# Kernel optimization log

Measured on AMD Instinct MI355X. Metric: run time of the kernel, lower is better.

The kernel has to match this reference:

```python
import jax, jax.numpy as jnp
import numpy as np

B, S, D_MODEL, H = 2, 2048, 768, 12
HD = D_MODEL // H  # head_dim = 64
EPS = 1e-5


def setup_inputs() -> dict:
    key = jax.random.key(0)
    ks = jax.random.split(key, 5)
    sc = 0.02
    return {
        "x": jax.random.normal(ks[0], (B, S, D_MODEL), dtype=jnp.float32),
        "Wproj_w": jax.random.normal(ks[1], (7 * D_MODEL, D_MODEL), dtype=jnp.float32) * sc,
        "Wproj_b": jax.random.normal(ks[2], (7 * D_MODEL,), dtype=jnp.float32) * sc,
        "gn_w": jnp.ones((D_MODEL,), dtype=jnp.float32),
        "gn_b": jnp.zeros((D_MODEL,), dtype=jnp.float32),
        "out_w": jax.random.normal(ks[3], (D_MODEL, D_MODEL), dtype=jnp.float32) * sc,
        "out_b": jax.random.normal(ks[4], (D_MODEL,), dtype=jnp.float32) * sc,
    }


def _time_swiglu(qkv):
    # qkv: [B, S, 7, H, D]
    q1, k1, q2, k2, q3, k3, v = [qkv[:, :, i] for i in range(7)]
    a1 = jnp.einsum('bthd,bshd->bhts', q1, k1)  # [B,H,S,S], raw scores, no softmax
    a2 = jnp.einsum('bthd,bshd->bhts', q2, k2)
    a3 = jnp.einsum('bthd,bshd->bhts', q3, k3)
    t1 = jax.nn.silu(jnp.einsum('bhts,bshd->bthd', a1, v))
    t2 = jnp.einsum('bhts,bshd->bthd', a2, v)
    return jnp.einsum('bhts,bshd->bthd', a3, t1 * t2)  # [B,S,H,D]


def _group_norm(ctx, gn_w, gn_b):
    # ctx: [B, S, D_MODEL]; torch applies GroupNorm(H, D_MODEL) over (B, C=D_MODEL, L=S)
    g = ctx.reshape(B, S, H, HD)
    mean = jnp.mean(g, axis=(1, 3), keepdims=True)          # per (batch, group) over (S, HD)
    var = jnp.var(g, axis=(1, 3), keepdims=True)
    g = (g - mean) * jax.lax.rsqrt(var + EPS)
    g = g.reshape(B, S, D_MODEL)
    return g * gn_w + gn_b


def reference(x, Wproj_w, Wproj_b, gn_w, gn_b, out_w, out_b):
    qkv = x @ Wproj_w.T + Wproj_b                  # [B,S,7*D_MODEL]
    qkv = qkv.reshape(B, S, 7, H, HD)
    ctx = _time_swiglu(qkv).reshape(B, S, D_MODEL)  # [B,S,D_MODEL]
    ctx = _group_norm(ctx, gn_w, gn_b)
    return ctx @ out_w.T + out_b
```

## Files before the change

kernel.cpp:

```cpp
#include <hip/hip_runtime.h>
#include <hip/hip_bf16.h>
#include <stdint.h>

typedef short short8 __attribute__((ext_vector_type(8)));
typedef float f32x4 __attribute__((ext_vector_type(4)));
typedef float f32x16 __attribute__((ext_vector_type(16)));
typedef unsigned short u16x4 __attribute__((ext_vector_type(4)));
typedef unsigned uint4v __attribute__((ext_vector_type(4)));

#define MFMA16 __builtin_amdgcn_mfma_f32_16x16x32_bf16
#define MFMA32 __builtin_amdgcn_mfma_f32_32x32x16_bf16

typedef unsigned int __attribute__((address_space(1))) as1_u32;
typedef unsigned int __attribute__((address_space(3))) as3_u32;
#define GLOAD16(gsrc, ldst) \
  __builtin_amdgcn_global_load_lds((const as1_u32*)(gsrc), (as3_u32*)(ldst), 16, 0, 0)

__device__ __forceinline__ unsigned short f2bf(float f) {
  __hip_bfloat16 h = __float2bfloat16(f);
  return *(unsigned short*)&h;
}
__device__ __forceinline__ unsigned pk2(float lo, float hi) {
  return ((unsigned)f2bf(hi) << 16) | (unsigned)f2bf(lo);
}
__device__ __forceinline__ void plswap(unsigned &a, unsigned &b) {
  asm volatile("v_permlane32_swap_b32 %0, %1" : "+v"(a), "+v"(b));
}

__device__ __forceinline__ short8 pv_frag(const f32x16* acc, int kc2) {
  int n = kc2 >> 1, c = kc2 & 1;
  int o0 = 2 * c, o1 = 2 * c + 1;
  unsigned x0 = pk2(acc[n][o0 * 4 + 0], acc[n][o0 * 4 + 1]);
  unsigned x1 = pk2(acc[n][o0 * 4 + 2], acc[n][o0 * 4 + 3]);
  unsigned y0 = pk2(acc[n][o1 * 4 + 0], acc[n][o1 * 4 + 1]);
  unsigned y1 = pk2(acc[n][o1 * 4 + 2], acc[n][o1 * 4 + 3]);
  plswap(x0, y0);
  plswap(x1, y1);
  uint4v fu; fu.x = x0; fu.y = x1; fu.z = y0; fu.w = y1;
  return __builtin_bit_cast(short8, fu);
}

__global__ __launch_bounds__(256) void cvt_bf16_4(const float* __restrict__ in,
                                                  unsigned short* __restrict__ out,
                                                  int n) {
  int i = (blockIdx.x * 256 + threadIdx.x) * 4;
  if (i >= n) return;
  f32x4 v = *(const f32x4*)(in + i);
  u16x4 o;
  o.x = f2bf(v.x); o.y = f2bf(v.y); o.z = f2bf(v.z); o.w = f2bf(v.w);
  *(u16x4*)(out + i) = o;
}

__global__ __launch_bounds__(256) void transp64(const unsigned short* __restrict__ src,
                                                int stride, int off,
                                                unsigned short* __restrict__ dst) {
  __shared__ __align__(16) unsigned short t[64 * 64];
  const int tid = threadIdx.x;
  const int tt = blockIdx.x, bh = blockIdx.y;
  const int b = bh / 12, h = bh % 12;
  const unsigned short* sbase = src + (size_t)(b * 2048 + tt * 64) * stride + h * 64 + off;
  for (int it = 0; it < 2; ++it) {
    int slot = it * 256 + tid, s = slot >> 3, j = slot & 7;
    short8 v = *(const short8*)(sbase + (size_t)s * stride + j * 8);
    int phys = (s + 8 * j) & 63;
    for (int e = 0; e < 8; ++e)
      t[(j * 8 + e) * 64 + phys] = ((unsigned short*)&v)[e];
  }
  __syncthreads();
  unsigned short* dbase = dst + (size_t)bh * 64 * 2048 + tt * 64;
  for (int it = 0; it < 2; ++it) {
    int slot = it * 256 + tid, d = slot >> 3, c = slot & 7;
    int pc = (c + (d >> 3)) & 7;
    short8 v = *(const short8*)(t + d * 64 + pc * 8);
    *(short8*)(dbase + (size_t)d * 2048 + c * 8) = v;
  }
}

template <bool OUT_BF16>
__global__ __launch_bounds__(256) void gemm_nt(const unsigned short* __restrict__ A,
                                               const unsigned short* __restrict__ Bm,
                                               const float* __restrict__ bias,
                                               void* __restrict__ Cout,
                                               int M, int N, int K) {
  __shared__ __align__(16) char smem[32768];
  char* As = smem;
  char* Bs = smem + 16384;
  const int tid = threadIdx.x;
  const int w = tid >> 6, l = tid & 63;
  const int wm = w >> 1, wn = w & 1;
  const int Row0 = blockIdx.y * 128, Col0 = blockIdx.x * 128;

  f32x4 z; z.x = 0.f; z.y = 0.f; z.z = 0.f; z.w = 0.f;
  f32x4 acc[4][4];
  for (int m = 0; m < 4; ++m)
    for (int n = 0; n < 4; ++n) acc[m][n] = z;

  for (int k0 = 0; k0 < K; k0 += 64) {
    for (int it = 0; it < 4; ++it) {
      int slot = it * 256 + tid;
      int row = slot >> 3, j = slot & 7;
      int gc = j ^ (row & 7);
      GLOAD16(A + (size_t)(Row0 + row) * K + k0 + gc * 8, As + slot * 16);
      GLOAD16(Bm + (size_t)(Col0 + row) * K + k0 + gc * 8, Bs + slot * 16);
    }
    __syncthreads();
    for (int kc = 0; kc < 2; ++kc) {
      int c = (l >> 4) + 4 * kc;
      short8 af[4], bf[4];
      for (int m = 0; m < 4; ++m) {
        int t = wm * 64 + m * 16 + (l & 15);
        af[m] = *(const short8*)(As + t * 128 + ((c ^ (t & 7)) * 16));
      }
      for (int n = 0; n < 4; ++n) {
        int t = wn * 64 + n * 16 + (l & 15);
        bf[n] = *(const short8*)(Bs + t * 128 + ((c ^ (t & 7)) * 16));
      }
      for (int m = 0; m < 4; ++m)
        for (int n = 0; n < 4; ++n)
          acc[m][n] = MFMA16(af[m], bf[n], acc[m][n], 0, 0, 0);
    }
    __syncthreads();
  }
  for (int n = 0; n < 4; ++n) {
    int col = Col0 + wn * 64 + n * 16 + (l & 15);
    float bv = bias[col];
    for (int m = 0; m < 4; ++m) {
      int rbase = Row0 + wm * 64 + m * 16 + (l >> 4) * 4;
      for (int r = 0; r < 4; ++r) {
        float v = acc[m][n][r] + bv;
        size_t idx = (size_t)(rbase + r) * N + col;
        if (OUT_BF16) ((unsigned short*)Cout)[idx] = f2bf(v);
        else          ((float*)Cout)[idx] = v;
      }
    }
  }
}

__global__ __launch_bounds__(256) void pass1(const unsigned short* __restrict__ qkv,
                                             const unsigned short* __restrict__ vt,
                                             unsigned short* __restrict__ u) {
  __shared__ __align__(16) char smem[24576];
  char* K1s = smem;
  char* K2s = smem + 8192;
  char* Vts = smem + 16384;
  const int tid = threadIdx.x, w = tid >> 6, l = tid & 63;
  const int g5 = l >> 5, l31 = l & 31;
  const int tt = blockIdx.x, bh = blockIdx.y;
  const int b = bh / 12, h = bh % 12;

  const int tg = tt * 128 + w * 32 + l31;
  const unsigned short* qrow = qkv + (size_t)(b * 2048 + tg) * 5376 + h * 64;
  short8 q1f[4], q2f[4];
#pragma unroll
  for (int kc = 0; kc < 4; ++kc) {
    int d = kc * 16 + g5 * 8;
    q1f[kc] = *(const short8*)(qrow + 0 * 768 + d);
    q2f[kc] = *(const short8*)(qrow + 2 * 768 + d);
  }

  f32x16 z16;
#pragma unroll
  for (int i = 0; i < 16; ++i) z16[i] = 0.f;
  f32x16 t1a[2], t2a[2];
  t1a[0] = z16; t1a[1] = z16; t2a[0] = z16; t2a[1] = z16;

  for (int s0 = 0; s0 < 2048; s0 += 64) {
#pragma unroll
    for (int it = 0; it < 2; ++it) {
      int slot = it * 256 + tid;
      int row = slot >> 3, j = slot & 7;
      int gc = j ^ (row & 7);
      const unsigned short* ksrc =
          qkv + (size_t)(b * 2048 + s0 + row) * 5376 + h * 64 + 768 + gc * 8;
      GLOAD16(ksrc, K1s + slot * 16);
      GLOAD16(ksrc + 2 * 768, K2s + slot * 16);
      GLOAD16(vt + (size_t)(bh * 64 + row) * 2048 + s0 + gc * 8, Vts + slot * 16);
    }
    __syncthreads();

    f32x16 a1t[2], a2t[2];
    a1t[0] = z16; a1t[1] = z16; a2t[0] = z16; a2t[1] = z16;
#pragma unroll
    for (int kc = 0; kc < 4; ++kc) {
#pragma unroll
      for (int n = 0; n < 2; ++n) {
        int srow = n * 32 + l31;
        int off = srow * 128 + (((kc * 2 + g5) ^ (l31 & 7)) * 16);
        a1t[n] = MFMA32(*(const short8*)(K1s + off), q1f[kc], a1t[n], 0, 0, 0);
        a2t[n] = MFMA32(*(const short8*)(K2s + off), q2f[kc], a2t[n], 0, 0, 0);
      }
    }

#pragma unroll
    for (int kc2 = 0; kc2 < 4; ++kc2) {
      short8 pa1 = pv_frag(a1t, kc2);
      short8 pa2 = pv_frag(a2t, kc2);
#pragma unroll
      for (int dn = 0; dn < 2; ++dn) {
        int drow = dn * 32 + l31;
        short8 vf = *(const short8*)(Vts + drow * 128 + (((kc2 * 2 + g5) ^ (l31 & 7)) * 16));
        t1a[dn] = MFMA32(pa1, vf, t1a[dn], 0, 0, 0);
        t2a[dn] = MFMA32(pa2, vf, t2a[dn], 0, 0, 0);
      }
    }
    __syncthreads();
  }

#pragma unroll
  for (int dn = 0; dn < 2; ++dn)
#pragma unroll
    for (int r = 0; r < 16; ++r) {
      int t = tt * 128 + w * 32 + (r & 3) + 8 * (r >> 2) + 4 * g5;
      int d = dn * 32 + l31;
      float x1 = t1a[dn][r], x2 = t2a[dn][r];
      float uu = (x1 / (1.f + expf(-x1))) * x2;
      u[(size_t)(b * 2048 + t) * 768 + h * 64 + d] = f2bf(uu);
    }
}

__global__ __launch_bounds__(256) void pass2(const unsigned short* __restrict__ qkv,
                                             const unsigned short* __restrict__ ut,
                                             float* __restrict__ ctx,
                                             float* __restrict__ partials) {
  __shared__ __align__(16) char smem[16384];
  char* K3s = smem;
  char* Uts = smem + 8192;
  const int tid = threadIdx.x, w = tid >> 6, l = tid & 63;
  const int g5 = l >> 5, l31 = l & 31;
  const int tt = blockIdx.x, bh = blockIdx.y;
  const int b = bh / 12, h = bh % 12;

  const int tg = tt * 128 + w * 32 + l31;
  const unsigned short* qrow = qkv + (size_t)(b * 2048 + tg) * 5376 + h * 64;
  short8 q3f[4];
#pragma unroll
  for (int kc = 0; kc < 4; ++kc)
    q3f[kc] = *(const short8*)(qrow + 4 * 768 + kc * 16 + g5 * 8);

  f32x16 z16;
#pragma unroll
  for (int i = 0; i < 16; ++i) z16[i] = 0.f;
  f32x16 ca[2];
  ca[0] = z16; ca[1] = z16;

  for (int s0 = 0; s0 < 2048; s0 += 64) {
#pragma unroll
    for (int it = 0; it < 2; ++it) {
      int slot = it * 256 + tid;
      int row = slot >> 3, j = slot & 7;
      int gc = j ^ (row & 7);
      GLOAD16(qkv + (size_t)(b * 2048 + s0 + row) * 5376 + h * 64 + 5 * 768 + gc * 8,
              K3s + slot * 16);
      GLOAD16(ut + (size_t)(bh * 64 + row) * 2048 + s0 + gc * 8, Uts + slot * 16);
    }
    __syncthreads();

    f32x16 a3t[2];
    a3t[0] = z16; a3t[1] = z16;
#pragma unroll
    for (int kc = 0; kc < 4; ++kc) {
#pragma unroll
      for (int n = 0; n < 2; ++n) {
        int srow = n * 32 + l31;
        int off = srow * 128 + (((kc * 2 + g5) ^ (l31 & 7)) * 16);
        a3t[n] = MFMA32(*(const short8*)(K3s + off), q3f[kc], a3t[n], 0, 0, 0);
      }
    }
#pragma unroll
    for (int kc2 = 0; kc2 < 4; ++kc2) {
      short8 pa = pv_frag(a3t, kc2);
#pragma unroll
      for (int dn = 0; dn < 2; ++dn) {
        int drow = dn * 32 + l31;
        short8 uf = *(const short8*)(Uts + drow * 128 + (((kc2 * 2 + g5) ^ (l31 & 7)) * 16));
        ca[dn] = MFMA32(pa, uf, ca[dn], 0, 0, 0);
      }
    }
    __syncthreads();
  }

  float psum = 0.f, psum2 = 0.f;
#pragma unroll
  for (int dn = 0; dn < 2; ++dn)
#pragma unroll
    for (int r = 0; r < 16; ++r) {
      int t = tt * 128 + w * 32 + (r & 3) + 8 * (r >> 2) + 4 * g5;
      int d = dn * 32 + l31;
      float v = ca[dn][r];
      ctx[(size_t)(b * 2048 + t) * 768 + h * 64 + d] = v;
      psum += v; psum2 += v * v;
    }

  float* red = (float*)smem;
  red[tid] = psum; red[256 + tid] = psum2;
  __syncthreads();
  for (int st = 128; st > 0; st >>= 1) {
    if (tid < st) {
      red[tid] += red[tid + st];
      red[256 + tid] += red[256 + tid + st];
    }
    __syncthreads();
  }
  if (tid == 0) {
    partials[(bh * 16 + tt) * 2] = red[0];
    partials[(bh * 16 + tt) * 2 + 1] = red[256];
  }
}

__global__ __launch_bounds__(64) void gn_finalize(const float* __restrict__ partials,
                                                  float* __restrict__ stats) {
  const int g = blockIdx.x;
  const int l = threadIdx.x;
  double s = 0.0, s2 = 0.0;
  if (l < 16) {
    s = (double)partials[(g * 16 + l) * 2];
    s2 = (double)partials[(g * 16 + l) * 2 + 1];
  }
  for (int off = 32; off > 0; off >>= 1) {
    s += __shfl_down(s, off, 64);
    s2 += __shfl_down(s2, off, 64);
  }
  if (l == 0) {
    const double N = 2048.0 * 64.0;
    double mean = s / N;
    double var = s2 / N - mean * mean;
    stats[g * 2] = (float)mean;
    stats[g * 2 + 1] = (float)(1.0 / sqrt(var + 1e-5));
  }
}

__global__ __launch_bounds__(256) void gn_apply(const float* __restrict__ ctx,
                                                const float* __restrict__ stats,
                                                const float* __restrict__ gw,
                                                const float* __restrict__ gb,
                                                unsigned short* __restrict__ outc) {
  int i = blockIdx.x * 256 + threadIdx.x;
  if (i >= 4096 * 768) return;
  int c = i % 768;
  int b = i / (2048 * 768);
  int g = b * 12 + (c >> 6);
  float v = (ctx[i] - stats[2 * g]) * stats[2 * g + 1];
  outc[i] = f2bf(v * gw[c] + gb[c]);
}

extern "C" void kernel_launch(void* const* d_in, const int* in_sizes, int n_in,
                              void* d_out, int out_size, void* d_ws, size_t ws_size,
                              hipStream_t stream) {
  const float* x   = (const float*)d_in[0];
  const float* Wpw = (const float*)d_in[1];
  const float* Wpb = (const float*)d_in[2];
  const float* gnw = (const float*)d_in[3];
  const float* gnb = (const float*)d_in[4];
  const float* ow  = (const float*)d_in[5];
  const float* ob  = (const float*)d_in[6];
  float* out = (float*)d_out;

  char* ws = (char*)d_ws;
  size_t off = 0;
  auto carve = [&](size_t bytes) {
    char* p = ws + off;
    off = (off + bytes + 255) & ~(size_t)255;
    return p;
  };
  unsigned short* xb   = (unsigned short*)carve((size_t)4096 * 768 * 2);
  unsigned short* wb   = (unsigned short*)carve((size_t)5376 * 768 * 2);
  unsigned short* owb  = (unsigned short*)carve((size_t)768 * 768 * 2);
  unsigned short* qkvb = (unsigned short*)carve((size_t)4096 * 5376 * 2);
  unsigned short* ub   = (unsigned short*)carve((size_t)4096 * 768 * 2);
  unsigned short* vtb  = (unsigned short*)carve((size_t)24 * 64 * 2048 * 2);
  unsigned short* utb  = (unsigned short*)carve((size_t)24 * 64 * 2048 * 2);
  float* ctx           = (float*)carve((size_t)4096 * 768 * 4);
  float* partials      = (float*)carve(24 * 16 * 2 * 4);
  float* stats         = (float*)carve(48 * 4);

  cvt_bf16_4<<<3072, 256, 0, stream>>>(x, xb, 4096 * 768);
  cvt_bf16_4<<<4032, 256, 0, stream>>>(Wpw, wb, 5376 * 768);
  cvt_bf16_4<<<576, 256, 0, stream>>>(ow, owb, 768 * 768);

  gemm_nt<true><<<dim3(42, 32), 256, 0, stream>>>(xb, wb, Wpb, qkvb, 4096, 5376, 768);
  transp64<<<dim3(32, 24), 256, 0, stream>>>(qkvb, 5376, 6 * 768, vtb);
  pass1<<<dim3(16, 24), 256, 0, stream>>>(qkvb, vtb, ub);
  transp64<<<dim3(32, 24), 256, 0, stream>>>(ub, 768, 0, utb);
  pass2<<<dim3(16, 24), 256, 0, stream>>>(qkvb, utb, ctx, partials);
  gn_finalize<<<24, 64, 0, stream>>>(partials, stats);
  gn_apply<<<12288, 256, 0, stream>>>(ctx, stats, gnw, gnb, xb);
  gemm_nt<false><<<dim3(6, 32), 256, 0, stream>>>(xb, owb, ob, out, 4096, 768, 768);
}
```

Before: 233.3 us.

## Split sequence reduction across two wave groups in pass1 and pass2

Doubles the block size of the two attention passes to 512 threads. Each half of the block processes one half of the key/sequence range with its own LDS staging buffers, and the partial accumulators are then combined through shared memory before the epilogue. The grid has only 384 blocks, so this is meant to put more waves per CU and hide latency on the long serial s-loop. The cost is extra LDS use, more barriers, an accumulator merge step, and half the waves sitting idle during the epilogue.

```diff
diff --git a/kernel.cpp b/kernel.cpp
--- a/kernel.cpp
+++ b/kernel.cpp
@@ -136,19 +136,21 @@
   }
 }
 
-__global__ __launch_bounds__(256) void pass1(const unsigned short* __restrict__ qkv,
-                                             const unsigned short* __restrict__ vt,
-                                             unsigned short* __restrict__ u) {
-  __shared__ __align__(16) char smem[24576];
-  char* K1s = smem;
-  char* K2s = smem + 8192;
-  char* Vts = smem + 16384;
+__global__ __launch_bounds__(512, 4) void pass1(const unsigned short* __restrict__ qkv,
+                                                const unsigned short* __restrict__ vt,
+                                                unsigned short* __restrict__ u) {
+  __shared__ __align__(16) char smem[49152];
   const int tid = threadIdx.x, w = tid >> 6, l = tid & 63;
+  const int sh = w >> 2, wi = w & 3;
+  const int tidh = tid & 255;
   const int g5 = l >> 5, l31 = l & 31;
   const int tt = blockIdx.x, bh = blockIdx.y;
   const int b = bh / 12, h = bh % 12;
-
-  const int tg = tt * 128 + w * 32 + l31;
+  char* K1s = smem + sh * 24576;
+  char* K2s = K1s + 8192;
+  char* Vts = K1s + 16384;
+
+  const int tg = tt * 128 + wi * 32 + l31;
   const unsigned short* qrow = qkv + (size_t)(b * 2048 + tg) * 5376 + h * 64;
   short8 q1f[4], q2f[4];
 #pragma unroll
@@ -164,10 +166,11 @@
   f32x16 t1a[2], t2a[2];
   t1a[0] = z16; t1a[1] = z16; t2a[0] = z16; t2a[1] = z16;
 
-  for (int s0 = 0; s0 < 2048; s0 += 64) {
+  for (int si = 0; si < 16; ++si) {
+    const int s0 = sh * 1024 + si * 64;
 #pragma unroll
     for (int it = 0; it < 2; ++it) {
-      int slot = it * 256 + tid;
+      int slot = it * 256 + tidh;
       int row = slot >> 3, j = slot & 7;
       int gc = j ^ (row & 7);
       const unsigned short* ksrc =
@@ -206,31 +209,79 @@
     __syncthreads();
   }
 
-#pragma unroll
-  for (int dn = 0; dn < 2; ++dn)
-#pragma unroll
-    for (int r = 0; r < 16; ++r) {
-      int t = tt * 128 + w * 32 + (r & 3) + 8 * (r >> 2) + 4 * g5;
-      int d = dn * 32 + l31;
-      float x1 = t1a[dn][r], x2 = t2a[dn][r];
-      float uu = (x1 / (1.f + expf(-x1))) * x2;
-      u[(size_t)(b * 2048 + t) * 768 + h * 64 + d] = f2bf(uu);
-    }
-}
-
-__global__ __launch_bounds__(256) void pass2(const unsigned short* __restrict__ qkv,
-                                             const unsigned short* __restrict__ ut,
-                                             float* __restrict__ ctx,
-                                             float* __restrict__ partials) {
-  __shared__ __align__(16) char smem[16384];
-  char* K3s = smem;
-  char* Uts = smem + 8192;
+  char* comb = smem + wi * 8192;
+  if (sh == 1) {
+#pragma unroll
+    for (int c = 0; c < 8; ++c) {
+      f32x4 q;
+      q.x = t1a[c >> 2][(c & 3) * 4 + 0];
+      q.y = t1a[c >> 2][(c & 3) * 4 + 1];
+      q.z = t1a[c >> 2][(c & 3) * 4 + 2];
+      q.w = t1a[c >> 2][(c & 3) * 4 + 3];
+      *(f32x4*)(comb + c * 1024 + l * 16) = q;
+    }
+  }
+  __syncthreads();
+  if (sh == 0) {
+#pragma unroll
+    for (int c = 0; c < 8; ++c) {
+      f32x4 q = *(const f32x4*)(comb + c * 1024 + l * 16);
+      t1a[c >> 2][(c & 3) * 4 + 0] += q.x;
+      t1a[c >> 2][(c & 3) * 4 + 1] += q.y;
+      t1a[c >> 2][(c & 3) * 4 + 2] += q.z;
+      t1a[c >> 2][(c & 3) * 4 + 3] += q.w;
+    }
+  }
+  __syncthreads();
+  if (sh == 1) {
+#pragma unroll
+    for (int c = 0; c < 8; ++c) {
+      f32x4 q;
+      q.x = t2a[c >> 2][(c & 3) * 4 + 0];
+      q.y = t2a[c >> 2][(c & 3) * 4 + 1];
+      q.z = t2a[c >> 2][(c & 3) * 4 + 2];
+      q.w = t2a[c >> 2][(c & 3) * 4 + 3];
+      *(f32x4*)(comb + c * 1024 + l * 16) = q;
+    }
+  }
+  __syncthreads();
+  if (sh == 0) {
+#pragma unroll
+    for (int c = 0; c < 8; ++c) {
+      f32x4 q = *(const f32x4*)(comb + c * 1024 + l * 16);
+      t2a[c >> 2][(c & 3) * 4 + 0] += q.x;
+      t2a[c >> 2][(c & 3) * 4 + 1] += q.y;
+      t2a[c >> 2][(c & 3) * 4 + 2] += q.z;
+      t2a[c >> 2][(c & 3) * 4 + 3] += q.w;
+    }
+#pragma unroll
+    for (int dn = 0; dn < 2; ++dn)
+#pragma unroll
+      for (int r = 0; r < 16; ++r) {
+        int t = tt * 128 + wi * 32 + (r & 3) + 8 * (r >> 2) + 4 * g5;
+        int d = dn * 32 + l31;
+        float x1 = t1a[dn][r], x2 = t2a[dn][r];
+        float uu = (x1 / (1.f + expf(-x1))) * x2;
+        u[(size_t)(b * 2048 + t) * 768 + h * 64 + d] = f2bf(uu);
+      }
+  }
+}
+
+__global__ __launch_bounds__(512, 4) void pass2(const unsigned short* __restrict__ qkv,
+                                                const unsigned short* __restrict__ ut,
+                                                float* __restrict__ ctx,
+                                                float* __restrict__ partials) {
+  __shared__ __align__(16) char smem[32768];
   const int tid = threadIdx.x, w = tid >> 6, l = tid & 63;
+  const int sh = w >> 2, wi = w & 3;
+  const int tidh = tid & 255;
   const int g5 = l >> 5, l31 = l & 31;
   const int tt = blockIdx.x, bh = blockIdx.y;
   const int b = bh / 12, h = bh % 12;
-
-  const int tg = tt * 128 + w * 32 + l31;
+  char* K3s = smem + sh * 16384;
+  char* Uts = K3s + 8192;
+
+  const int tg = tt * 128 + wi * 32 + l31;
   const unsigned short* qrow = qkv + (size_t)(b * 2048 + tg) * 5376 + h * 64;
   short8 q3f[4];
 #pragma unroll
@@ -243,10 +294,11 @@
   f32x16 ca[2];
   ca[0] = z16; ca[1] = z16;
 
-  for (int s0 = 0; s0 < 2048; s0 += 64) {
+  for (int si = 0; si < 16; ++si) {
+    const int s0 = sh * 1024 + si * 64;
 #pragma unroll
     for (int it = 0; it < 2; ++it) {
-      int slot = it * 256 + tid;
+      int slot = it * 256 + tidh;
       int row = slot >> 3, j = slot & 7;
       int gc = j ^ (row & 7);
       GLOAD16(qkv + (size_t)(b * 2048 + s0 + row) * 5376 + h * 64 + 5 * 768 + gc * 8,
@@ -279,31 +331,55 @@
     __syncthreads();
   }
 
+  char* comb = smem + wi * 8192;
+  if (sh == 1) {
+#pragma unroll
+    for (int c = 0; c < 8; ++c) {
+      f32x4 q;
+      q.x = ca[c >> 2][(c & 3) * 4 + 0];
+      q.y = ca[c >> 2][(c & 3) * 4 + 1];
+      q.z = ca[c >> 2][(c & 3) * 4 + 2];
+      q.w = ca[c >> 2][(c & 3) * 4 + 3];
+      *(f32x4*)(comb + c * 1024 + l * 16) = q;
+    }
+  }
+  __syncthreads();
   float psum = 0.f, psum2 = 0.f;
-#pragma unroll
-  for (int dn = 0; dn < 2; ++dn)
-#pragma unroll
-    for (int r = 0; r < 16; ++r) {
-      int t = tt * 128 + w * 32 + (r & 3) + 8 * (r >> 2) + 4 * g5;
-      int d = dn * 32 + l31;
-      float v = ca[dn][r];
-      ctx[(size_t)(b * 2048 + t) * 768 + h * 64 + d] = v;
-      psum += v; psum2 += v * v;
-    }
+  if (sh == 0) {
+#pragma unroll
+    for (int c = 0; c < 8; ++c) {
+      f32x4 q = *(const f32x4*)(comb + c * 1024 + l * 16);
+      ca[c >> 2][(c & 3) * 4 + 0] += q.x;
+      ca[c >> 2][(c & 3) * 4 + 1] += q.y;
+      ca[c >> 2][(c & 3) * 4 + 2] += q.z;
+      ca[c >> 2][(c & 3) * 4 + 3] += q.w;
+    }
+#pragma unroll
+    for (int dn = 0; dn < 2; ++dn)
+#pragma unroll
+      for (int r = 0; r < 16; ++r) {
+        int t = tt * 128 + wi * 32 + (r & 3) + 8 * (r >> 2) + 4 * g5;
+        int d = dn * 32 + l31;
+        float v = ca[dn][r];
+        ctx[(size_t)(b * 2048 + t) * 768 + h * 64 + d] = v;
+        psum += v; psum2 += v * v;
+      }
+  }
+  __syncthreads();
 
   float* red = (float*)smem;
-  red[tid] = psum; red[256 + tid] = psum2;
-  __syncthreads();
-  for (int st = 128; st > 0; st >>= 1) {
+  red[tid] = psum; red[512 + tid] = psum2;
+  __syncthreads();
+  for (int st = 256; st > 0; st >>= 1) {
     if (tid < st) {
       red[tid] += red[tid + st];
-      red[256 + tid] += red[256 + tid + st];
+      red[512 + tid] += red[512 + tid + st];
     }
     __syncthreads();
   }
   if (tid == 0) {
     partials[(bh * 16 + tt) * 2] = red[0];
-    partials[(bh * 16 + tt) * 2 + 1] = red[256];
+    partials[(bh * 16 + tt) * 2 + 1] = red[512];
   }
 }
 
@@ -379,9 +455,9 @@
 
   gemm_nt<true><<<dim3(42, 32), 256, 0, stream>>>(xb, wb, Wpb, qkvb, 4096, 5376, 768);
   transp64<<<dim3(32, 24), 256, 0, stream>>>(qkvb, 5376, 6 * 768, vtb);
-  pass1<<<dim3(16, 24), 256, 0, stream>>>(qkvb, vtb, ub);
+  pass1<<<dim3(16, 24), 512, 0, stream>>>(qkvb, vtb, ub);
   transp64<<<dim3(32, 24), 256, 0, stream>>>(ub, 768, 0, utb);
-  pass2<<<dim3(16, 24), 256, 0, stream>>>(qkvb, utb, ctx, partials);
+  pass2<<<dim3(16, 24), 512, 0, stream>>>(qkvb, utb, ctx, partials);
   gn_finalize<<<24, 64, 0, stream>>>(partials, stats);
   gn_apply<<<12288, 256, 0, stream>>>(ctx, stats, gnw, gnb, xb);
   gemm_nt<false><<<dim3(6, 32), 256, 0, stream>>>(xb, owb, ob, out, 4096, 768, 768);
```

New measurement: 321.9 us. 1.38x slower.

## Double-buffer K/V tiles and re-split attention passes into smaller 2-wave blocks

Applied to the files above, without the earlier changes.

Both attention passes now use 128-thread blocks over 64-row query tiles, doubling the grid from 384 to 768 blocks. In pass1 each wave owns one score matrix (q1/k1 or q2/k2) and the two halves are combined through shared memory before the SiLU product. In pass2 the two waves split the output head dimension. K and V tiles are double-buffered so the next tile's global-to-LDS loads overlap the current tile's MFMAs. This targets low occupancy and exposed load latency, at the cost of more LDS per block and an extra shared-memory exchange in pass1.

```diff
diff --git a/kernel.cpp b/kernel.cpp
--- a/kernel.cpp
+++ b/kernel.cpp
@@ -136,106 +136,136 @@
   }
 }
 
-__global__ __launch_bounds__(256) void pass1(const unsigned short* __restrict__ qkv,
+__global__ __launch_bounds__(128) void pass1(const unsigned short* __restrict__ qkv,
                                              const unsigned short* __restrict__ vt,
                                              unsigned short* __restrict__ u) {
-  __shared__ __align__(16) char smem[24576];
-  char* K1s = smem;
-  char* K2s = smem + 8192;
-  char* Vts = smem + 16384;
+  __shared__ __align__(16) char smem[49152];
   const int tid = threadIdx.x, w = tid >> 6, l = tid & 63;
   const int g5 = l >> 5, l31 = l & 31;
   const int tt = blockIdx.x, bh = blockIdx.y;
   const int b = bh / 12, h = bh % 12;
-
-  const int tg = tt * 128 + w * 32 + l31;
-  const unsigned short* qrow = qkv + (size_t)(b * 2048 + tg) * 5376 + h * 64;
-  short8 q1f[4], q2f[4];
-#pragma unroll
-  for (int kc = 0; kc < 4; ++kc) {
-    int d = kc * 16 + g5 * 8;
-    q1f[kc] = *(const short8*)(qrow + 0 * 768 + d);
-    q2f[kc] = *(const short8*)(qrow + 2 * 768 + d);
+  const int matOff = (w == 0) ? 0 : 2 * 768;
+
+  short8 qf[2][4];
+#pragma unroll
+  for (int tc = 0; tc < 2; ++tc) {
+    const unsigned short* qrow =
+        qkv + (size_t)(b * 2048 + tt * 64 + tc * 32 + l31) * 5376 + h * 64 + matOff;
+#pragma unroll
+    for (int kc = 0; kc < 4; ++kc)
+      qf[tc][kc] = *(const short8*)(qrow + kc * 16 + g5 * 8);
   }
 
   f32x16 z16;
 #pragma unroll
   for (int i = 0; i < 16; ++i) z16[i] = 0.f;
-  f32x16 t1a[2], t2a[2];
-  t1a[0] = z16; t1a[1] = z16; t2a[0] = z16; t2a[1] = z16;
-
-  for (int s0 = 0; s0 < 2048; s0 += 64) {
-#pragma unroll
-    for (int it = 0; it < 2; ++it) {
-      int slot = it * 256 + tid;
-      int row = slot >> 3, j = slot & 7;
-      int gc = j ^ (row & 7);
-      const unsigned short* ksrc =
-          qkv + (size_t)(b * 2048 + s0 + row) * 5376 + h * 64 + 768 + gc * 8;
-      GLOAD16(ksrc, K1s + slot * 16);
-      GLOAD16(ksrc + 2 * 768, K2s + slot * 16);
-      GLOAD16(vt + (size_t)(bh * 64 + row) * 2048 + s0 + gc * 8, Vts + slot * 16);
-    }
-    __syncthreads();
-
-    f32x16 a1t[2], a2t[2];
-    a1t[0] = z16; a1t[1] = z16; a2t[0] = z16; a2t[1] = z16;
-#pragma unroll
-    for (int kc = 0; kc < 4; ++kc) {
-#pragma unroll
-      for (int n = 0; n < 2; ++n) {
-        int srow = n * 32 + l31;
-        int off = srow * 128 + (((kc * 2 + g5) ^ (l31 & 7)) * 16);
-        a1t[n] = MFMA32(*(const short8*)(K1s + off), q1f[kc], a1t[n], 0, 0, 0);
-        a2t[n] = MFMA32(*(const short8*)(K2s + off), q2f[kc], a2t[n], 0, 0, 0);
-      }
-    }
-
+  f32x16 tacc[2][2];
+  tacc[0][0] = z16; tacc[0][1] = z16; tacc[1][0] = z16; tacc[1][1] = z16;
+
+  auto STAGE = [&](char* buf, int s0) {
+#pragma unroll
+    for (int c = 0; c < 4; ++c) {
+      int r = c * 128 + tid, row = r >> 3, j = r & 7, gc = j ^ (row & 7);
+      GLOAD16(qkv + (size_t)(b * 2048 + s0 + row) * 5376 + h * 64 + 1 * 768 + gc * 8,
+              buf + r * 16);
+    }
+#pragma unroll
+    for (int c = 0; c < 4; ++c) {
+      int r = c * 128 + tid, row = r >> 3, j = r & 7, gc = j ^ (row & 7);
+      GLOAD16(qkv + (size_t)(b * 2048 + s0 + row) * 5376 + h * 64 + 3 * 768 + gc * 8,
+              buf + 8192 + r * 16);
+    }
+#pragma unroll
+    for (int c = 0; c < 4; ++c) {
+      int r = c * 128 + tid, row = r >> 3, j = r & 7, gc = j ^ (row & 7);
+      GLOAD16(vt + (size_t)(bh * 64 + row) * 2048 + s0 + gc * 8, buf + 16384 + r * 16);
+    }
+  };
+
+  STAGE(smem, 0);
+  __syncthreads();
+  for (int si = 0; si < 32; ++si) {
+    char* cur = smem + (si & 1) * 24576;
+    if (si < 31) STAGE(smem + ((si + 1) & 1) * 24576, (si + 1) * 64);
+    const char* Ks = cur + w * 8192;
+    const char* Vs = cur + 16384;
+
+    f32x16 at[2][2];
+    at[0][0] = z16; at[0][1] = z16; at[1][0] = z16; at[1][1] = z16;
+#pragma unroll
+    for (int kc = 0; kc < 4; ++kc)
+#pragma unroll
+      for (int sn = 0; sn < 2; ++sn) {
+        int srow = sn * 32 + l31;
+        short8 kf = *(const short8*)(Ks + srow * 128 + (((kc * 2 + g5) ^ (l31 & 7)) * 16));
+        at[0][sn] = MFMA32(kf, qf[0][kc], at[0][sn], 0, 0, 0);
+        at[1][sn] = MFMA32(kf, qf[1][kc], at[1][sn], 0, 0, 0);
+      }
 #pragma unroll
     for (int kc2 = 0; kc2 < 4; ++kc2) {
-      short8 pa1 = pv_frag(a1t, kc2);
-      short8 pa2 = pv_frag(a2t, kc2);
+      short8 pa0 = pv_frag(at[0], kc2);
+      short8 pa1 = pv_frag(at[1], kc2);
 #pragma unroll
       for (int dn = 0; dn < 2; ++dn) {
         int drow = dn * 32 + l31;
-        short8 vf = *(const short8*)(Vts + drow * 128 + (((kc2 * 2 + g5) ^ (l31 & 7)) * 16));
-        t1a[dn] = MFMA32(pa1, vf, t1a[dn], 0, 0, 0);
-        t2a[dn] = MFMA32(pa2, vf, t2a[dn], 0, 0, 0);
+        short8 vf = *(const short8*)(Vs + drow * 128 + (((kc2 * 2 + g5) ^ (l31 & 7)) * 16));
+        tacc[0][dn] = MFMA32(pa0, vf, tacc[0][dn], 0, 0, 0);
+        tacc[1][dn] = MFMA32(pa1, vf, tacc[1][dn], 0, 0, 0);
       }
     }
     __syncthreads();
   }
 
-#pragma unroll
-  for (int dn = 0; dn < 2; ++dn)
-#pragma unroll
-    for (int r = 0; r < 16; ++r) {
-      int t = tt * 128 + w * 32 + (r & 3) + 8 * (r >> 2) + 4 * g5;
-      int d = dn * 32 + l31;
-      float x1 = t1a[dn][r], x2 = t2a[dn][r];
-      float uu = (x1 / (1.f + expf(-x1))) * x2;
-      u[(size_t)(b * 2048 + t) * 768 + h * 64 + d] = f2bf(uu);
-    }
-}
-
-__global__ __launch_bounds__(256) void pass2(const unsigned short* __restrict__ qkv,
+  float* exch = (float*)smem;
+  if (w == 1) {
+#pragma unroll
+    for (int tc = 0; tc < 2; ++tc)
+#pragma unroll
+      for (int dn = 0; dn < 2; ++dn)
+#pragma unroll
+        for (int r = 0; r < 16; ++r) {
+          int trow = tc * 32 + (r & 3) + 8 * (r >> 2) + 4 * g5;
+          exch[trow * 64 + dn * 32 + l31] = tacc[tc][dn][r];
+        }
+  }
+  __syncthreads();
+  if (w == 0) {
+#pragma unroll
+    for (int tc = 0; tc < 2; ++tc)
+#pragma unroll
+      for (int dn = 0; dn < 2; ++dn)
+#pragma unroll
+        for (int r = 0; r < 16; ++r) {
+          int crow = (r & 3) + 8 * (r >> 2) + 4 * g5;
+          int t = tt * 64 + tc * 32 + crow;
+          int d = dn * 32 + l31;
+          float x1 = tacc[tc][dn][r];
+          float x2 = exch[(tc * 32 + crow) * 64 + d];
+          float uu = (x1 / (1.f + expf(-x1))) * x2;
+          u[(size_t)(b * 2048 + t) * 768 + h * 64 + d] = f2bf(uu);
+        }
+  }
+}
+
+__global__ __launch_bounds__(128) void pass2(const unsigned short* __restrict__ qkv,
                                              const unsigned short* __restrict__ ut,
                                              float* __restrict__ ctx,
                                              float* __restrict__ partials) {
-  __shared__ __align__(16) char smem[16384];
-  char* K3s = smem;
-  char* Uts = smem + 8192;
+  __shared__ __align__(16) char smem[32768];
   const int tid = threadIdx.x, w = tid >> 6, l = tid & 63;
   const int g5 = l >> 5, l31 = l & 31;
   const int tt = blockIdx.x, bh = blockIdx.y;
   const int b = bh / 12, h = bh % 12;
 
-  const int tg = tt * 128 + w * 32 + l31;
-  const unsigned short* qrow = qkv + (size_t)(b * 2048 + tg) * 5376 + h * 64;
-  short8 q3f[4];
-#pragma unroll
-  for (int kc = 0; kc < 4; ++kc)
-    q3f[kc] = *(const short8*)(qrow + 4 * 768 + kc * 16 + g5 * 8);
+  short8 qf[2][4];
+#pragma unroll
+  for (int tc = 0; tc < 2; ++tc) {
+    const unsigned short* qrow =
+        qkv + (size_t)(b * 2048 + tt * 64 + tc * 32 + l31) * 5376 + h * 64 + 4 * 768;
+#pragma unroll
+    for (int kc = 0; kc < 4; ++kc)
+      qf[tc][kc] = *(const short8*)(qrow + kc * 16 + g5 * 8);
+  }
 
   f32x16 z16;
 #pragma unroll
@@ -243,67 +273,76 @@
   f32x16 ca[2];
   ca[0] = z16; ca[1] = z16;
 
-  for (int s0 = 0; s0 < 2048; s0 += 64) {
-#pragma unroll
-    for (int it = 0; it < 2; ++it) {
-      int slot = it * 256 + tid;
-      int row = slot >> 3, j = slot & 7;
-      int gc = j ^ (row & 7);
+  auto STAGE = [&](char* buf, int s0) {
+#pragma unroll
+    for (int c = 0; c < 4; ++c) {
+      int r = c * 128 + tid, row = r >> 3, j = r & 7, gc = j ^ (row & 7);
       GLOAD16(qkv + (size_t)(b * 2048 + s0 + row) * 5376 + h * 64 + 5 * 768 + gc * 8,
-              K3s + slot * 16);
-      GLOAD16(ut + (size_t)(bh * 64 + row) * 2048 + s0 + gc * 8, Uts + slot * 16);
+              buf + r * 16);
+    }
+#pragma unroll
+    for (int c = 0; c < 4; ++c) {
+      int r = c * 128 + tid, row = r >> 3, j = r & 7, gc = j ^ (row & 7);
+      GLOAD16(ut + (size_t)(bh * 64 + row) * 2048 + s0 + gc * 8, buf + 8192 + r * 16);
+    }
+  };
+
+  STAGE(smem, 0);
+  __syncthreads();
+  for (int si = 0; si < 32; ++si) {
+    char* cur = smem + (si & 1) * 16384;
+    if (si < 31) STAGE(smem + ((si + 1) & 1) * 16384, (si + 1) * 64);
+    const char* Ks = cur;
+    const char* Us = cur + 8192;
+
+    f32x16 at[2][2];
+    at[0][0] = z16; at[0][1] = z16; at[1][0] = z16; at[1][1] = z16;
+#pragma unroll
+    for (int kc = 0; kc < 4; ++kc)
+#pragma unroll
+      for (int sn = 0; sn < 2; ++sn) {
+        int srow = sn * 32 + l31;
+        short8 kf = *(const short8*)(Ks + srow * 128 + (((kc * 2 + g5) ^ (l31 & 7)) * 16));
+        at[0][sn] = MFMA32(kf, qf[0][kc], at[0][sn], 0, 0, 0);
+        at[1][sn] = MFMA32(kf, qf[1][kc], at[1][sn], 0, 0, 0);
+      }
+#pragma unroll
+    for (int kc2 = 0; kc2 < 4; ++kc2) {
+      short8 pa0 = pv_frag(at[0], kc2);
+      short8 pa1 = pv_frag(at[1], kc2);
+      int drow = w * 32 + l31;
+      short8 uf = *(const short8*)(Us + drow * 128 + (((kc2 * 2 + g5) ^ (l31 & 7)) * 16));
+      ca[0] = MFMA32(pa0, uf, ca[0], 0, 0, 0);
+      ca[1] = MFMA32(pa1, uf, ca[1], 0, 0, 0);
     }
     __syncthreads();
-
-    f32x16 a3t[2];
-    a3t[0] = z16; a3t[1] = z16;
-#pragma unroll
-    for (int kc = 0; kc < 4; ++kc) {
-#pragma unroll
-      for (int n = 0; n < 2; ++n) {
-        int srow = n * 32 + l31;
-        int off = srow * 128 + (((kc * 2 + g5) ^ (l31 & 7)) * 16);
-        a3t[n] = MFMA32(*(const short8*)(K3s + off), q3f[kc], a3t[n], 0, 0, 0);
-      }
-    }
-#pragma unroll
-    for (int kc2 = 0; kc2 < 4; ++kc2) {
-      short8 pa = pv_frag(a3t, kc2);
-#pragma unroll
-      for (int dn = 0; dn < 2; ++dn) {
-        int drow = dn * 32 + l31;
-        short8 uf = *(const short8*)(Uts + drow * 128 + (((kc2 * 2 + g5) ^ (l31 & 7)) * 16));
-        ca[dn] = MFMA32(pa, uf, ca[dn], 0, 0, 0);
-      }
-    }
-    __syncthreads();
   }
 
   float psum = 0.f, psum2 = 0.f;
 #pragma unroll
-  for (int dn = 0; dn < 2; ++dn)
+  for (int tc = 0; tc < 2; ++tc)
 #pragma unroll
     for (int r = 0; r < 16; ++r) {
-      int t = tt * 128 + w * 32 + (r & 3) + 8 * (r >> 2) + 4 * g5;
-      int d = dn * 32 + l31;
-      float v = ca[dn][r];
+      int t = tt * 64 + tc * 32 + (r & 3) + 8 * (r >> 2) + 4 * g5;
+      int d = w * 32 + l31;
+      float v = ca[tc][r];
       ctx[(size_t)(b * 2048 + t) * 768 + h * 64 + d] = v;
       psum += v; psum2 += v * v;
     }
 
   float* red = (float*)smem;
-  red[tid] = psum; red[256 + tid] = psum2;
+  red[tid] = psum; red[128 + tid] = psum2;
   __syncthreads();
-  for (int st = 128; st > 0; st >>= 1) {
+  for (int st = 64; st > 0; st >>= 1) {
     if (tid < st) {
       red[tid] += red[tid + st];
-      red[256 + tid] += red[256 + tid + st];
+      red[128 + tid] += red[128 + tid + st];
     }
     __syncthreads();
   }
   if (tid == 0) {
-    partials[(bh * 16 + tt) * 2] = red[0];
-    partials[(bh * 16 + tt) * 2 + 1] = red[256];
+    partials[(bh * 32 + tt) * 2] = red[0];
+    partials[(bh * 32 + tt) * 2 + 1] = red[128];
   }
 }
 
@@ -312,9 +351,9 @@
   const int g = blockIdx.x;
   const int l = threadIdx.x;
   double s = 0.0, s2 = 0.0;
-  if (l < 16) {
-    s = (double)partials[(g * 16 + l) * 2];
-    s2 = (double)partials[(g * 16 + l) * 2 + 1];
+  if (l < 32) {
+    s = (double)partials[(g * 32 + l) * 2];
+    s2 = (double)partials[(g * 32 + l) * 2 + 1];
   }
   for (int off = 32; off > 0; off >>= 1) {
     s += __shfl_down(s, off, 64);
@@ -370,7 +409,7 @@
   unsigned short* vtb  = (unsigned short*)carve((size_t)24 * 64 * 2048 * 2);
   unsigned short* utb  = (unsigned short*)carve((size_t)24 * 64 * 2048 * 2);
   float* ctx           = (float*)carve((size_t)4096 * 768 * 4);
-  float* partials      = (float*)carve(24 * 16 * 2 * 4);
+  float* partials      = (float*)carve(24 * 32 * 2 * 4);
   float* stats         = (float*)carve(48 * 4);
 
   cvt_bf16_4<<<3072, 256, 0, stream>>>(x, xb, 4096 * 768);
@@ -379,9 +418,9 @@
 
   gemm_nt<true><<<dim3(42, 32), 256, 0, stream>>>(xb, wb, Wpb, qkvb, 4096, 5376, 768);
   transp64<<<dim3(32, 24), 256, 0, stream>>>(qkvb, 5376, 6 * 768, vtb);
-  pass1<<<dim3(16, 24), 256, 0, stream>>>(qkvb, vtb, ub);
+  pass1<<<dim3(32, 24), 128, 0, stream>>>(qkvb, vtb, ub);
   transp64<<<dim3(32, 24), 256, 0, stream>>>(ub, 768, 0, utb);
-  pass2<<<dim3(16, 24), 256, 0, stream>>>(qkvb, utb, ctx, partials);
+  pass2<<<dim3(32, 24), 128, 0, stream>>>(qkvb, utb, ctx, partials);
   gn_finalize<<<24, 64, 0, stream>>>(partials, stats);
   gn_apply<<<12288, 256, 0, stream>>>(ctx, stats, gnw, gnb, xb);
   gemm_nt<false><<<dim3(6, 32), 256, 0, stream>>>(xb, owb, ob, out, 4096, 768, 768);
```

Result: slower. 241.2 us (+3.4%).
